# Kernel optimization log

Measured on AMD Instinct MI355X. Metric: run time of the kernel, lower is better.

## Reference

```python
import jax, jax.numpy as jnp
import numpy as np

T, B, N, C = 4, 16, 256, 512
H = 8
HID = 4 * C
TAU = 2.0
EPS = 1e-5
SCALE = 0.125

@jax.custom_vjp
def spike_fn(x):
    return (x >= 0.0).astype(x.dtype)

def _spike_fwd(x):
    return spike_fn(x), x

def _spike_bwd(x, g):
    alpha = 4.0  # spikingjelly sigmoid surrogate default
    s = jax.nn.sigmoid(alpha * x)
    return (g * alpha * s * (1.0 - s),)

spike_fn.defvjp(_spike_fwd, _spike_bwd)

def lif(x_seq, v_th=1.0):
    # Multi-step LIF: v += (x - v)/tau (decay_input, v_reset=0), hard reset, detach_reset
    def step(v, xt):
        v = v + (xt - v) / TAU
        s = spike_fn(v - v_th)
        v = v * (1.0 - jax.lax.stop_gradient(s))
        return v, s
    _, out = jax.lax.scan(step, jnp.zeros_like(x_seq[0]), x_seq)
    return out

def lin_bn(x2d, w, b, g, beta):
    # Linear then BatchNorm1d (training mode, per-channel stats over all rows).
    # BN on (TB, Cout, N) over (batch, N) == BN on flattened (TB*N, Cout) over axis 0.
    y = x2d @ w.T + b
    mu = jnp.mean(y, axis=0)
    var = jnp.var(y, axis=0)
    return g * (y - mu) * jax.lax.rsqrt(var + EPS) + beta

def setup_inputs() -> dict:
    key = jax.random.key(0)
    ks = jax.random.split(key, 10)
    d = {
        "x": jax.random.normal(ks[0], (T, B, N, C), jnp.float32),
        "s_x": jax.random.normal(ks[1], (T, B, N, C), jnp.float32),
    }
    def lin(k, cout, cin):
        return jax.random.normal(k, (cout, cin), jnp.float32) * 0.02
    d["qw"] = lin(ks[2], C, C); d["qb"] = jnp.zeros((C,), jnp.float32)
    d["qg"] = jnp.ones((C,), jnp.float32); d["qbeta"] = jnp.zeros((C,), jnp.float32)
    d["kw"] = lin(ks[3], C, C); d["kb"] = jnp.zeros((C,), jnp.float32)
    d["kg"] = jnp.ones((C,), jnp.float32); d["kbeta"] = jnp.zeros((C,), jnp.float32)
    d["vw"] = lin(ks[4], C, C); d["vb"] = jnp.zeros((C,), jnp.float32)
    d["vg"] = jnp.ones((C,), jnp.float32); d["vbeta"] = jnp.zeros((C,), jnp.float32)
    d["pw"] = lin(ks[5], C, C); d["pb"] = jnp.zeros((C,), jnp.float32)
    d["pg"] = jnp.ones((C,), jnp.float32); d["pbeta"] = jnp.zeros((C,), jnp.float32)
    d["f1w"] = lin(ks[6], HID, C); d["f1b"] = jnp.zeros((HID,), jnp.float32)
    d["f1g"] = jnp.ones((HID,), jnp.float32); d["f1beta"] = jnp.zeros((HID,), jnp.float32)
    d["f2w"] = lin(ks[7], C, HID); d["f2b"] = jnp.zeros((C,), jnp.float32)
    d["f2g"] = jnp.ones((C,), jnp.float32); d["f2beta"] = jnp.zeros((C,), jnp.float32)
    return d

def _block(x, s_x, qw, qb, qg, qbeta, kw, kb, kg, kbeta, vw, vb, vg, vbeta,
           pw, pb, pg, pbeta, f1w, f1b, f1g, f1beta, f2w, f2b, f2g, f2beta):
    Dh = C // H
    xf = x.reshape(T * B * N, C)
    # SSA (s_x is unused in the source forward)
    q = lif(lin_bn(xf, qw, qb, qg, qbeta).reshape(T, B, N, C))
    k = lif(lin_bn(xf, kw, kb, kg, kbeta).reshape(T, B, N, C))
    v = lin_bn(xf, vw, vb, vg, vbeta).reshape(T, B, N, C)  # v has no LIF in source
    q = q.reshape(T, B, N, H, Dh).transpose(0, 1, 3, 2, 4)  # tbhnd
    k = k.reshape(T, B, N, H, Dh).transpose(0, 1, 3, 2, 4)
    v = v.reshape(T, B, N, H, Dh).transpose(0, 1, 3, 2, 4)
    attn = jnp.einsum('tbhnd,tbhmd->tbhnm', q, k) * SCALE  # no softmax
    o = jnp.einsum('tbhnm,tbhmd->tbhnd', attn, v)
    o = o.transpose(0, 1, 3, 2, 4).reshape(T * B * N, C)
    o = lin_bn(o, pw, pb, pg, pbeta).reshape(T, B, N, C)
    x = x + o
    # MLP
    xf2 = x.reshape(T * B * N, C)
    h = lif(lin_bn(xf2, f1w, f1b, f1g, f1beta).reshape(T, B, N, HID))
    m = lif(lin_bn(h.reshape(T * B * N, HID), f2w, f2b, f2g, f2beta).reshape(T, B, N, C))
    return x + m

def reference(x, s_x, qw, qb, qg, qbeta, kw, kb, kg, kbeta, vw, vb, vg, vbeta,
              pw, pb, pg, pbeta, f1w, f1b, f1g, f1beta, f2w, f2b, f2g, f2beta):
    return _block(x, s_x, qw, qb, qg, qbeta, kw, kb, kg, kbeta, vw, vb, vg, vbeta,
                  pw, pb, pg, pbeta, f1w, f1b, f1g, f1beta, f2w, f2b, f2g, f2beta)
```

## Files before the change

kernel.cpp:

```cpp
#include <hip/hip_runtime.h>
#include <cstdint>

#define T_ 4
#define B_ 16
#define N_ 256
#define C_ 512
#define H_ 8
#define HID_ 2048
#define M_ (T_*B_*N_)
#define BNP_ (B_*N_)

__global__ __launch_bounds__(256, 2)
void gemm_f32_t128(const float* __restrict__ A, const float* __restrict__ W,
                   const float* __restrict__ bias, float* __restrict__ Y,
                   int Nc, int K) {
  __shared__ float As[2][16][132];
  __shared__ float Ws[2][16][132];
  const int tid  = threadIdx.x;
  const int row0 = blockIdx.y * 128;
  const int col0 = blockIdx.x * 128;
  const int tx = tid & 15, ty = tid >> 4;
  const int ar = tid >> 2;
  const int ac = (tid & 3) << 2;

  float acc[8][8];
  #pragma unroll
  for (int i = 0; i < 8; ++i)
    #pragma unroll
    for (int j = 0; j < 8; ++j) acc[i][j] = 0.f;

  const float* Ap0 = A + (size_t)(row0 + ar) * K + ac;
  const float* Ap1 = A + (size_t)(row0 + ar + 64) * K + ac;
  const float* Wp0 = W + (size_t)(col0 + ar) * K + ac;
  const float* Wp1 = W + (size_t)(col0 + ar + 64) * K + ac;

  float4 pa0 = *(const float4*)Ap0;
  float4 pa1 = *(const float4*)Ap1;
  float4 pw0 = *(const float4*)Wp0;
  float4 pw1 = *(const float4*)Wp1;
  As[0][ac+0][ar] = pa0.x; As[0][ac+1][ar] = pa0.y; As[0][ac+2][ar] = pa0.z; As[0][ac+3][ar] = pa0.w;
  As[0][ac+0][ar+64] = pa1.x; As[0][ac+1][ar+64] = pa1.y; As[0][ac+2][ar+64] = pa1.z; As[0][ac+3][ar+64] = pa1.w;
  Ws[0][ac+0][ar] = pw0.x; Ws[0][ac+1][ar] = pw0.y; Ws[0][ac+2][ar] = pw0.z; Ws[0][ac+3][ar] = pw0.w;
  Ws[0][ac+0][ar+64] = pw1.x; Ws[0][ac+1][ar+64] = pw1.y; Ws[0][ac+2][ar+64] = pw1.z; Ws[0][ac+3][ar+64] = pw1.w;
  __syncthreads();

  int buf = 0;
  for (int k0 = 0; k0 < K; k0 += 16) {
    const bool last = (k0 + 16 >= K);
    if (!last) {
      pa0 = *(const float4*)(Ap0 + k0 + 16);
      pa1 = *(const float4*)(Ap1 + k0 + 16);
      pw0 = *(const float4*)(Wp0 + k0 + 16);
      pw1 = *(const float4*)(Wp1 + k0 + 16);
    }
    #pragma unroll
    for (int kk = 0; kk < 16; ++kk) {
      float a[8], b[8];
      *(float4*)&a[0] = *(const float4*)&As[buf][kk][ty*4];
      *(float4*)&a[4] = *(const float4*)&As[buf][kk][64 + ty*4];
      *(float4*)&b[0] = *(const float4*)&Ws[buf][kk][tx*4];
      *(float4*)&b[4] = *(const float4*)&Ws[buf][kk][64 + tx*4];
      #pragma unroll
      for (int i = 0; i < 8; ++i)
        #pragma unroll
        for (int j = 0; j < 8; ++j)
          acc[i][j] = fmaf(a[i], b[j], acc[i][j]);
    }
    if (!last) {
      int nb = buf ^ 1;
      As[nb][ac+0][ar] = pa0.x; As[nb][ac+1][ar] = pa0.y; As[nb][ac+2][ar] = pa0.z; As[nb][ac+3][ar] = pa0.w;
      As[nb][ac+0][ar+64] = pa1.x; As[nb][ac+1][ar+64] = pa1.y; As[nb][ac+2][ar+64] = pa1.z; As[nb][ac+3][ar+64] = pa1.w;
      Ws[nb][ac+0][ar] = pw0.x; Ws[nb][ac+1][ar] = pw0.y; Ws[nb][ac+2][ar] = pw0.z; Ws[nb][ac+3][ar] = pw0.w;
      Ws[nb][ac+0][ar+64] = pw1.x; Ws[nb][ac+1][ar+64] = pw1.y; Ws[nb][ac+2][ar+64] = pw1.z; Ws[nb][ac+3][ar+64] = pw1.w;
      __syncthreads();
      buf = nb;
    }
  }

  #pragma unroll
  for (int ih = 0; ih < 2; ++ih)
    #pragma unroll
    for (int i = 0; i < 4; ++i) {
      size_t r = (size_t)(row0 + ih*64 + ty*4 + i);
      #pragma unroll
      for (int jh = 0; jh < 2; ++jh) {
        int c = col0 + jh*64 + tx*4;
        float4 o4;
        o4.x = acc[ih*4+i][jh*4+0] + bias[c+0];
        o4.y = acc[ih*4+i][jh*4+1] + bias[c+1];
        o4.z = acc[ih*4+i][jh*4+2] + bias[c+2];
        o4.w = acc[ih*4+i][jh*4+3] + bias[c+3];
        *(float4*)(Y + r * Nc + c) = o4;
      }
    }
}

__global__ __launch_bounds__(256)
void gemm_f32_t64x128(const float* __restrict__ A, const float* __restrict__ W,
                      const float* __restrict__ bias, float* __restrict__ Y,
                      int Nc, int K) {
  __shared__ float As[2][16][68];
  __shared__ float Ws[2][16][132];
  const int tid  = threadIdx.x;
  const int row0 = blockIdx.y * 64;
  const int col0 = blockIdx.x * 128;
  const int tx = tid & 15, ty = tid >> 4;
  const int ar = tid >> 2;
  const int ac = (tid & 3) << 2;

  float acc[4][8];
  #pragma unroll
  for (int i = 0; i < 4; ++i)
    #pragma unroll
    for (int j = 0; j < 8; ++j) acc[i][j] = 0.f;

  const float* Ap  = A + (size_t)(row0 + ar) * K + ac;
  const float* Wp0 = W + (size_t)(col0 + ar) * K + ac;
  const float* Wp1 = W + (size_t)(col0 + ar + 64) * K + ac;

  float4 pa  = *(const float4*)Ap;
  float4 pw0 = *(const float4*)Wp0;
  float4 pw1 = *(const float4*)Wp1;
  As[0][ac+0][ar] = pa.x; As[0][ac+1][ar] = pa.y; As[0][ac+2][ar] = pa.z; As[0][ac+3][ar] = pa.w;
  Ws[0][ac+0][ar] = pw0.x; Ws[0][ac+1][ar] = pw0.y; Ws[0][ac+2][ar] = pw0.z; Ws[0][ac+3][ar] = pw0.w;
  Ws[0][ac+0][ar+64] = pw1.x; Ws[0][ac+1][ar+64] = pw1.y; Ws[0][ac+2][ar+64] = pw1.z; Ws[0][ac+3][ar+64] = pw1.w;
  __syncthreads();

  int buf = 0;
  for (int k0 = 0; k0 < K; k0 += 16) {
    const bool last = (k0 + 16 >= K);
    if (!last) {
      pa  = *(const float4*)(Ap  + k0 + 16);
      pw0 = *(const float4*)(Wp0 + k0 + 16);
      pw1 = *(const float4*)(Wp1 + k0 + 16);
    }
    #pragma unroll
    for (int kk = 0; kk < 16; ++kk) {
      float4 av = *(const float4*)&As[buf][kk][ty*4];
      float b[8];
      *(float4*)&b[0] = *(const float4*)&Ws[buf][kk][tx*4];
      *(float4*)&b[4] = *(const float4*)&Ws[buf][kk][64 + tx*4];
      float a[4] = {av.x, av.y, av.z, av.w};
      #pragma unroll
      for (int i = 0; i < 4; ++i)
        #pragma unroll
        for (int j = 0; j < 8; ++j)
          acc[i][j] = fmaf(a[i], b[j], acc[i][j]);
    }
    if (!last) {
      int nb = buf ^ 1;
      As[nb][ac+0][ar] = pa.x; As[nb][ac+1][ar] = pa.y; As[nb][ac+2][ar] = pa.z; As[nb][ac+3][ar] = pa.w;
      Ws[nb][ac+0][ar] = pw0.x; Ws[nb][ac+1][ar] = pw0.y; Ws[nb][ac+2][ar] = pw0.z; Ws[nb][ac+3][ar] = pw0.w;
      Ws[nb][ac+0][ar+64] = pw1.x; Ws[nb][ac+1][ar+64] = pw1.y; Ws[nb][ac+2][ar+64] = pw1.z; Ws[nb][ac+3][ar+64] = pw1.w;
      __syncthreads();
      buf = nb;
    }
  }

  #pragma unroll
  for (int i = 0; i < 4; ++i) {
    size_t r = (size_t)(row0 + ty*4 + i);
    #pragma unroll
    for (int jh = 0; jh < 2; ++jh) {
      int c = col0 + jh*64 + tx*4;
      float4 o4;
      o4.x = acc[i][jh*4+0] + bias[c+0];
      o4.y = acc[i][jh*4+1] + bias[c+1];
      o4.z = acc[i][jh*4+2] + bias[c+2];
      o4.w = acc[i][jh*4+3] + bias[c+3];
      *(float4*)(Y + r * Nc + c) = o4;
    }
  }
}

__global__ __launch_bounds__(256)
void gemm_f64_v2(const float* __restrict__ A, const float* __restrict__ W,
                 const float* __restrict__ bias, float* __restrict__ Y,
                 int Nc, int K) {
  __shared__ double As[2][16][68];
  __shared__ double Ws[2][16][68];
  const int tid  = threadIdx.x;
  const int row0 = blockIdx.y * 64;
  const int col0 = blockIdx.x * 64;
  const int tx = tid & 15, ty = tid >> 4;
  const int lr = tid >> 2;
  const int lk = (tid & 3) << 2;

  double acc[4][4];
  #pragma unroll
  for (int i = 0; i < 4; ++i)
    #pragma unroll
    for (int j = 0; j < 4; ++j) acc[i][j] = 0.0;

  const float* Ap = A + (size_t)(row0 + lr) * K + lk;
  const float* Wp = W + (size_t)(col0 + lr) * K + lk;

  float4 pa = *(const float4*)Ap;
  float4 pw = *(const float4*)Wp;
  As[0][lk+0][lr] = (double)pa.x; As[0][lk+1][lr] = (double)pa.y;
  As[0][lk+2][lr] = (double)pa.z; As[0][lk+3][lr] = (double)pa.w;
  Ws[0][lk+0][lr] = (double)pw.x; Ws[0][lk+1][lr] = (double)pw.y;
  Ws[0][lk+2][lr] = (double)pw.z; Ws[0][lk+3][lr] = (double)pw.w;
  __syncthreads();

  int buf = 0;
  for (int k0 = 0; k0 < K; k0 += 16) {
    const bool last = (k0 + 16 >= K);
    if (!last) {
      pa = *(const float4*)(Ap + k0 + 16);
      pw = *(const float4*)(Wp + k0 + 16);
    }
    #pragma unroll
    for (int kk = 0; kk < 16; ++kk) {
      double a[4], b[4];
      *(double2*)&a[0] = *(const double2*)&As[buf][kk][ty*4];
      *(double2*)&a[2] = *(const double2*)&As[buf][kk][ty*4+2];
      *(double2*)&b[0] = *(const double2*)&Ws[buf][kk][tx*2];
      *(double2*)&b[2] = *(const double2*)&Ws[buf][kk][32 + tx*2];
      #pragma unroll
      for (int i = 0; i < 4; ++i)
        #pragma unroll
        for (int j = 0; j < 4; ++j)
          acc[i][j] = fma(a[i], b[j], acc[i][j]);
    }
    if (!last) {
      int nb = buf ^ 1;
      As[nb][lk+0][lr] = (double)pa.x; As[nb][lk+1][lr] = (double)pa.y;
      As[nb][lk+2][lr] = (double)pa.z; As[nb][lk+3][lr] = (double)pa.w;
      Ws[nb][lk+0][lr] = (double)pw.x; Ws[nb][lk+1][lr] = (double)pw.y;
      Ws[nb][lk+2][lr] = (double)pw.z; Ws[nb][lk+3][lr] = (double)pw.w;
      __syncthreads();
      buf = nb;
    }
  }

  #pragma unroll
  for (int i = 0; i < 4; ++i) {
    size_t r = (size_t)(row0 + ty*4 + i);
    int c0 = col0 + tx*2;
    float2 o0;
    o0.x = (float)(acc[i][0] + (double)bias[c0+0]);
    o0.y = (float)(acc[i][1] + (double)bias[c0+1]);
    *(float2*)(Y + r * Nc + c0) = o0;
    int c1 = col0 + 32 + tx*2;
    float2 o1;
    o1.x = (float)(acc[i][2] + (double)bias[c1+0]);
    o1.y = (float)(acc[i][3] + (double)bias[c1+1]);
    *(float2*)(Y + r * Nc + c1) = o1;
  }
}

__global__ __launch_bounds__(256)
void col_stats_partial(const float* __restrict__ Y, int Nc,
                       float* __restrict__ psum, float* __restrict__ psq) {
  const int r0 = blockIdx.x * 32;
  for (int c = threadIdx.x; c < Nc; c += 256) {
    float s = 0.f, q = 0.f;
    const float* p = Y + (size_t)r0 * Nc + c;
    for (int r = 0; r < 32; ++r) {
      float v = p[(size_t)r * Nc];
      s += v;
      q = fmaf(v, v, q);
    }
    psum[(size_t)blockIdx.x * Nc + c] = s;
    psq [(size_t)blockIdx.x * Nc + c] = q;
  }
}

__global__ void col_stats_final(const float* __restrict__ psum, const float* __restrict__ psq,
                                int Nc, const float* __restrict__ g, const float* __restrict__ beta,
                                float* __restrict__ chp) {
  int c = blockIdx.x * blockDim.x + threadIdx.x;
  if (c >= Nc) return;
  double s = 0.0, q = 0.0;
  for (int p = 0; p < 512; ++p) {
    s += (double)psum[(size_t)p * Nc + c];
    q += (double)psq [(size_t)p * Nc + c];
  }
  double mean = s / (double)M_;
  double var  = q / (double)M_ - mean * mean;
  float alpha = g[c] / sqrtf((float)var + 1e-5f);
  chp[2*c]   = alpha;
  chp[2*c+1] = fmaf(-(float)mean, alpha, beta[c]);
}

__global__ void col_stats_final_f64(const float* __restrict__ psum, const float* __restrict__ psq,
                                    int Nc, const float* __restrict__ g, const float* __restrict__ beta,
                                    double* __restrict__ chpd) {
  int c = blockIdx.x * blockDim.x + threadIdx.x;
  if (c >= Nc) return;
  double s = 0.0, q = 0.0;
  for (int p = 0; p < 512; ++p) {
    s += (double)psum[(size_t)p * Nc + c];
    q += (double)psq [(size_t)p * Nc + c];
  }
  double mean = s / (double)M_;
  double var  = q / (double)M_ - mean * mean;
  double alpha = (double)g[c] / sqrt(var + 1e-5);
  chpd[2*c]   = alpha;
  chpd[2*c+1] = (double)beta[c] - mean * alpha;
}

__global__ __launch_bounds__(256)
void bnlif_mask(const float* __restrict__ Y, const float* __restrict__ chp,
                unsigned long long* __restrict__ mask) {
  int lane = threadIdx.x & 63;
  int u  = blockIdx.x * 4 + (threadIdx.x >> 6);
  int bn = u >> 3, cg = u & 7;
  int c  = cg * 64 + lane;
  float alpha = chp[2*c], bb = chp[2*c+1];
  float v = 0.f;
  #pragma unroll
  for (int t = 0; t < 4; ++t) {
    float y  = Y[((size_t)(t * BNP_ + bn)) * C_ + c];
    float uu = fmaf(y, alpha, bb);
    v = v + (uu - v) * 0.5f;
    bool sp = (v >= 1.0f);
    unsigned long long m = __ballot(sp);
    if (sp) v = 0.f;
    if (lane == 0) mask[((size_t)(t * BNP_ + bn)) * H_ + cg] = m;
  }
}

__global__ void bn_apply_f64(const float* __restrict__ Y, const double* __restrict__ chpd,
                             float* __restrict__ out) {
  const long total4 = (long)M_ * C_ / 4;
  for (long i = (long)blockIdx.x * blockDim.x + threadIdx.x; i < total4;
       i += (long)gridDim.x * blockDim.x) {
    int c4 = (int)(i & (C_/4 - 1)) * 4;
    float4 y = ((const float4*)Y)[i];
    float4 r;
    r.x = (float)fma((double)y.x, chpd[2*(c4+0)], chpd[2*(c4+0)+1]);
    r.y = (float)fma((double)y.y, chpd[2*(c4+1)], chpd[2*(c4+1)+1]);
    r.z = (float)fma((double)y.z, chpd[2*(c4+2)], chpd[2*(c4+2)+1]);
    r.w = (float)fma((double)y.w, chpd[2*(c4+3)], chpd[2*(c4+3)+1]);
    ((float4*)out)[i] = r;
  }
}

__global__ void bn_residual_f64(const float* __restrict__ Y, const double* __restrict__ chpd,
                                const float* __restrict__ x, float* __restrict__ out) {
  const long total4 = (long)M_ * C_ / 4;
  for (long i = (long)blockIdx.x * blockDim.x + threadIdx.x; i < total4;
       i += (long)gridDim.x * blockDim.x) {
    int c4 = (int)(i & (C_/4 - 1)) * 4;
    float4 y = ((const float4*)Y)[i];
    float4 xv = ((const float4*)x)[i];
    float4 r;
    r.x = (float)((double)xv.x + fma((double)y.x, chpd[2*(c4+0)], chpd[2*(c4+0)+1]));
    r.y = (float)((double)xv.y + fma((double)y.y, chpd[2*(c4+1)], chpd[2*(c4+1)+1]));
    r.z = (float)((double)xv.z + fma((double)y.z, chpd[2*(c4+2)], chpd[2*(c4+2)+1]));
    r.w = (float)((double)xv.w + fma((double)y.w, chpd[2*(c4+3)], chpd[2*(c4+3)+1]));
    ((float4*)out)[i] = r;
  }
}

__global__ __launch_bounds__(256)
void bnlif_inplace(float* __restrict__ Y, const float* __restrict__ chp) {
  int c  = blockIdx.x * 256 + threadIdx.x;
  int bn = blockIdx.y;
  float alpha = chp[2*c], bb = chp[2*c+1];
  float v = 0.f;
  #pragma unroll
  for (int t = 0; t < 4; ++t) {
    size_t idx = ((size_t)(t * BNP_ + bn)) * HID_ + c;
    float uu = fmaf(Y[idx], alpha, bb);
    v = v + (uu - v) * 0.5f;
    bool sp = (v >= 1.f);
    Y[idx] = sp ? 1.f : 0.f;
    if (sp) v = 0.f;
  }
}

__global__ __launch_bounds__(256)
void bnlif_final(const float* __restrict__ Y, const float* __restrict__ chp,
                 const float* __restrict__ xo, float* __restrict__ out) {
  int c  = blockIdx.x * 256 + threadIdx.x;
  int bn = blockIdx.y;
  float alpha = chp[2*c], bb = chp[2*c+1];
  float v = 0.f;
  #pragma unroll
  for (int t = 0; t < 4; ++t) {
    size_t idx = ((size_t)(t * BNP_ + bn)) * C_ + c;
    float uu = fmaf(Y[idx], alpha, bb);
    v = v + (uu - v) * 0.5f;
    bool sp = (v >= 1.f);
    out[idx] = xo[idx] + (sp ? 1.f : 0.f);
    if (sp) v = 0.f;
  }
}

__global__ __launch_bounds__(256)
void attn_kernel_f64(const unsigned long long* __restrict__ qmask,
                     const unsigned long long* __restrict__ kmask,
                     const float* __restrict__ v, float* __restrict__ o) {
  __shared__ unsigned long long km[256];
  __shared__ float vt[256][64];
  int rb  = blockIdx.x & 3;
  int tbh = blockIdx.x >> 2;
  int h   = tbh & 7, tb = tbh >> 3;
  int tid = threadIdx.x;

  km[tid] = kmask[(size_t)(tb * 256 + tid) * H_ + h];
  const float* vbase = v + (size_t)tb * 256 * C_ + h * 64;
  #pragma unroll
  for (int i = 0; i < 16; ++i) {
    int f = i * 256 + tid;
    int r = f >> 4, c4 = f & 15;
    *(float4*)&vt[r][c4 * 4] = *(const float4*)(vbase + (size_t)r * C_ + c4 * 4);
  }
  int lane = tid & 63, w = tid >> 6;
  int nr = lane & 15, dg = lane >> 4;
  int n  = rb * 64 + w * 16 + nr;
  unsigned long long qm = qmask[(size_t)(tb * 256 + n) * H_ + h];
  __syncthreads();

  double acc[16];
  #pragma unroll
  for (int j = 0; j < 16; ++j) acc[j] = 0.0;

  for (int m = 0; m < 256; ++m) {
    double s = (double)__popcll(qm & km[m]) * 0.125;
    #pragma unroll
    for (int j = 0; j < 4; ++j) {
      float4 vv = *(const float4*)&vt[m][dg * 16 + j * 4];
      acc[j*4+0] = fma(s, (double)vv.x, acc[j*4+0]);
      acc[j*4+1] = fma(s, (double)vv.y, acc[j*4+1]);
      acc[j*4+2] = fma(s, (double)vv.z, acc[j*4+2]);
      acc[j*4+3] = fma(s, (double)vv.w, acc[j*4+3]);
    }
  }
  float* orow = o + (size_t)(tb * 256 + n) * C_ + h * 64 + dg * 16;
  #pragma unroll
  for (int j = 0; j < 4; ++j)
    *(float4*)(orow + j * 4) = make_float4((float)acc[j*4], (float)acc[j*4+1],
                                           (float)acc[j*4+2], (float)acc[j*4+3]);
}

extern "C" void kernel_launch(void* const* d_in, const int* in_sizes, int n_in,
                              void* d_out, int out_size, void* d_ws, size_t ws_size,
                              hipStream_t stream) {
  const float* x    = (const float*)d_in[0];
  const float* qw   = (const float*)d_in[2];
  const float* qb   = (const float*)d_in[3];
  const float* qg   = (const float*)d_in[4];
  const float* qbe  = (const float*)d_in[5];
  const float* kw   = (const float*)d_in[6];
  const float* kb   = (const float*)d_in[7];
  const float* kg   = (const float*)d_in[8];
  const float* kbe  = (const float*)d_in[9];
  const float* vw   = (const float*)d_in[10];
  const float* vb   = (const float*)d_in[11];
  const float* vg   = (const float*)d_in[12];
  const float* vbe  = (const float*)d_in[13];
  const float* pw   = (const float*)d_in[14];
  const float* pb   = (const float*)d_in[15];
  const float* pg   = (const float*)d_in[16];
  const float* pbe  = (const float*)d_in[17];
  const float* f1w  = (const float*)d_in[18];
  const float* f1b  = (const float*)d_in[19];
  const float* f1g  = (const float*)d_in[20];
  const float* f1be = (const float*)d_in[21];
  const float* f2w  = (const float*)d_in[22];
  const float* f2b  = (const float*)d_in[23];
  const float* f2g  = (const float*)d_in[24];
  const float* f2be = (const float*)d_in[25];

  char* ws = (char*)d_ws;
  float* bufY = (float*)(ws);
  float* bufV = (float*)(ws + 134217728ull);
  float* bufO = (float*)(ws + 167772160ull);
  unsigned long long* qmask = (unsigned long long*)(ws + 201326592ull);
  unsigned long long* kmask = (unsigned long long*)(ws + 202375168ull);
  float* psum = (float*)(ws + 203423744ull);
  float* psq  = (float*)(ws + 207618048ull);
  float* chp  = (float*)(ws + 211812352ull);
  double* chpd = (double*)(ws + 211828736ull);

  float* out = (float*)d_out;

  gemm_f32_t64x128<<<dim3(4,256), 256, 0, stream>>>(x, qw, qb, bufY, C_, C_);
  col_stats_partial<<<512, 256, 0, stream>>>(bufY, C_, psum, psq);
  col_stats_final<<<2, 256, 0, stream>>>(psum, psq, C_, qg, qbe, chp);
  bnlif_mask<<<8192, 256, 0, stream>>>(bufY, chp, qmask);
  gemm_f32_t64x128<<<dim3(4,256), 256, 0, stream>>>(x, kw, kb, bufY, C_, C_);
  col_stats_partial<<<512, 256, 0, stream>>>(bufY, C_, psum, psq);
  col_stats_final<<<2, 256, 0, stream>>>(psum, psq, C_, kg, kbe, chp);
  bnlif_mask<<<8192, 256, 0, stream>>>(bufY, chp, kmask);
  gemm_f64_v2<<<dim3(8,256), 256, 0, stream>>>(x, vw, vb, bufY, C_, C_);
  col_stats_partial<<<512, 256, 0, stream>>>(bufY, C_, psum, psq);
  col_stats_final_f64<<<2, 256, 0, stream>>>(psum, psq, C_, vg, vbe, chpd);
  bn_apply_f64<<<2048, 256, 0, stream>>>(bufY, chpd, bufV);
  attn_kernel_f64<<<2048, 256, 0, stream>>>(qmask, kmask, bufV, bufO);
  gemm_f64_v2<<<dim3(8,256), 256, 0, stream>>>(bufO, pw, pb, bufY, C_, C_);
  col_stats_partial<<<512, 256, 0, stream>>>(bufY, C_, psum, psq);
  col_stats_final_f64<<<2, 256, 0, stream>>>(psum, psq, C_, pg, pbe, chpd);
  bn_residual_f64<<<2048, 256, 0, stream>>>(bufY, chpd, x, bufO);
  gemm_f32_t128<<<dim3(16,128), 256, 0, stream>>>(bufO, f1w, f1b, bufY, HID_, C_);
  col_stats_partial<<<512, 256, 0, stream>>>(bufY, HID_, psum, psq);
  col_stats_final<<<8, 256, 0, stream>>>(psum, psq, HID_, f1g, f1be, chp);
  bnlif_inplace<<<dim3(8,4096), 256, 0, stream>>>(bufY, chp);
  gemm_f32_t64x128<<<dim3(4,256), 256, 0, stream>>>(bufY, f2w, f2b, bufV, C_, HID_);
  col_stats_partial<<<512, 256, 0, stream>>>(bufV, C_, psum, psq);
  col_stats_final<<<2, 256, 0, stream>>>(psum, psq, C_, f2g, f2be, chp);
  bnlif_final<<<dim3(2,4096), 256, 0, stream>>>(bufV, chp, bufO, out);
}
```

Measured before the change: 1.982 ms.

## Fuse Q/K projections into one GEMM and enlarge f64 and FC2 GEMM tiles

Q and K linear projections now run in a single kernel that loads each activation tile once and multiplies it against both weight matrices, writing two outputs. The f64 GEMM used for V and the projection is widened from a 64x64 to a 64x128 tile, and the FC2 GEMM moves to the 128x128 f32 kernel. The aim is to cut redundant activation reads and launches and raise arithmetic intensity. The cost is more registers and shared memory per block and fewer blocks, which can lower occupancy.

```diff
diff --git a/kernel.cpp b/kernel.cpp
--- a/kernel.cpp
+++ b/kernel.cpp
@@ -95,12 +95,15 @@
     }
 }
 
-__global__ __launch_bounds__(256)
-void gemm_f32_t64x128(const float* __restrict__ A, const float* __restrict__ W,
-                      const float* __restrict__ bias, float* __restrict__ Y,
-                      int Nc, int K) {
+__global__ __launch_bounds__(256, 2)
+void gemm_f32_qk(const float* __restrict__ A,
+                 const float* __restrict__ Wq, const float* __restrict__ bq,
+                 const float* __restrict__ Wk, const float* __restrict__ bk,
+                 float* __restrict__ Yq, float* __restrict__ Yk,
+                 int Nc, int K) {
   __shared__ float As[2][16][68];
-  __shared__ float Ws[2][16][132];
+  __shared__ float Wqs[2][16][132];
+  __shared__ float Wks[2][16][132];
   const int tid  = threadIdx.x;
   const int row0 = blockIdx.y * 64;
   const int col0 = blockIdx.x * 128;
@@ -108,22 +111,125 @@
   const int ar = tid >> 2;
   const int ac = (tid & 3) << 2;
 
-  float acc[4][8];
+  float accq[4][8], acck[4][8];
   #pragma unroll
   for (int i = 0; i < 4; ++i)
     #pragma unroll
-    for (int j = 0; j < 8; ++j) acc[i][j] = 0.f;
-
-  const float* Ap  = A + (size_t)(row0 + ar) * K + ac;
-  const float* Wp0 = W + (size_t)(col0 + ar) * K + ac;
-  const float* Wp1 = W + (size_t)(col0 + ar + 64) * K + ac;
+    for (int j = 0; j < 8; ++j) { accq[i][j] = 0.f; acck[i][j] = 0.f; }
+
+  const float* Ap   = A  + (size_t)(row0 + ar) * K + ac;
+  const float* Wqp0 = Wq + (size_t)(col0 + ar) * K + ac;
+  const float* Wqp1 = Wq + (size_t)(col0 + ar + 64) * K + ac;
+  const float* Wkp0 = Wk + (size_t)(col0 + ar) * K + ac;
+  const float* Wkp1 = Wk + (size_t)(col0 + ar + 64) * K + ac;
+
+  float4 pa  = *(const float4*)Ap;
+  float4 pq0 = *(const float4*)Wqp0;
+  float4 pq1 = *(const float4*)Wqp1;
+  float4 pk0 = *(const float4*)Wkp0;
+  float4 pk1 = *(const float4*)Wkp1;
+  As[0][ac+0][ar] = pa.x; As[0][ac+1][ar] = pa.y; As[0][ac+2][ar] = pa.z; As[0][ac+3][ar] = pa.w;
+  Wqs[0][ac+0][ar] = pq0.x; Wqs[0][ac+1][ar] = pq0.y; Wqs[0][ac+2][ar] = pq0.z; Wqs[0][ac+3][ar] = pq0.w;
+  Wqs[0][ac+0][ar+64] = pq1.x; Wqs[0][ac+1][ar+64] = pq1.y; Wqs[0][ac+2][ar+64] = pq1.z; Wqs[0][ac+3][ar+64] = pq1.w;
+  Wks[0][ac+0][ar] = pk0.x; Wks[0][ac+1][ar] = pk0.y; Wks[0][ac+2][ar] = pk0.z; Wks[0][ac+3][ar] = pk0.w;
+  Wks[0][ac+0][ar+64] = pk1.x; Wks[0][ac+1][ar+64] = pk1.y; Wks[0][ac+2][ar+64] = pk1.z; Wks[0][ac+3][ar+64] = pk1.w;
+  __syncthreads();
+
+  int buf = 0;
+  for (int k0 = 0; k0 < K; k0 += 16) {
+    const bool last = (k0 + 16 >= K);
+    if (!last) {
+      pa  = *(const float4*)(Ap   + k0 + 16);
+      pq0 = *(const float4*)(Wqp0 + k0 + 16);
+      pq1 = *(const float4*)(Wqp1 + k0 + 16);
+      pk0 = *(const float4*)(Wkp0 + k0 + 16);
+      pk1 = *(const float4*)(Wkp1 + k0 + 16);
+    }
+    #pragma unroll
+    for (int kk = 0; kk < 16; ++kk) {
+      float4 av = *(const float4*)&As[buf][kk][ty*4];
+      float a[4] = {av.x, av.y, av.z, av.w};
+      float b[8];
+      *(float4*)&b[0] = *(const float4*)&Wqs[buf][kk][tx*4];
+      *(float4*)&b[4] = *(const float4*)&Wqs[buf][kk][64 + tx*4];
+      #pragma unroll
+      for (int i = 0; i < 4; ++i)
+        #pragma unroll
+        for (int j = 0; j < 8; ++j)
+          accq[i][j] = fmaf(a[i], b[j], accq[i][j]);
+      *(float4*)&b[0] = *(const float4*)&Wks[buf][kk][tx*4];
+      *(float4*)&b[4] = *(const float4*)&Wks[buf][kk][64 + tx*4];
+      #pragma unroll
+      for (int i = 0; i < 4; ++i)
+        #pragma unroll
+        for (int j = 0; j < 8; ++j)
+          acck[i][j] = fmaf(a[i], b[j], acck[i][j]);
+    }
+    if (!last) {
+      int nb = buf ^ 1;
+      As[nb][ac+0][ar] = pa.x; As[nb][ac+1][ar] = pa.y; As[nb][ac+2][ar] = pa.z; As[nb][ac+3][ar] = pa.w;
+      Wqs[nb][ac+0][ar] = pq0.x; Wqs[nb][ac+1][ar] = pq0.y; Wqs[nb][ac+2][ar] = pq0.z; Wqs[nb][ac+3][ar] = pq0.w;
+      Wqs[nb][ac+0][ar+64] = pq1.x; Wqs[nb][ac+1][ar+64] = pq1.y; Wqs[nb][ac+2][ar+64] = pq1.z; Wqs[nb][ac+3][ar+64] = pq1.w;
+      Wks[nb][ac+0][ar] = pk0.x; Wks[nb][ac+1][ar] = pk0.y; Wks[nb][ac+2][ar] = pk0.z; Wks[nb][ac+3][ar] = pk0.w;
+      Wks[nb][ac+0][ar+64] = pk1.x; Wks[nb][ac+1][ar+64] = pk1.y; Wks[nb][ac+2][ar+64] = pk1.z; Wks[nb][ac+3][ar+64] = pk1.w;
+      __syncthreads();
+      buf = nb;
+    }
+  }
+
+  #pragma unroll
+  for (int i = 0; i < 4; ++i) {
+    size_t r = (size_t)(row0 + ty*4 + i);
+    #pragma unroll
+    for (int jh = 0; jh < 2; ++jh) {
+      int c = col0 + jh*64 + tx*4;
+      float4 oq, ok;
+      oq.x = accq[i][jh*4+0] + bq[c+0];
+      oq.y = accq[i][jh*4+1] + bq[c+1];
+      oq.z = accq[i][jh*4+2] + bq[c+2];
+      oq.w = accq[i][jh*4+3] + bq[c+3];
+      *(float4*)(Yq + r * Nc + c) = oq;
+      ok.x = acck[i][jh*4+0] + bk[c+0];
+      ok.y = acck[i][jh*4+1] + bk[c+1];
+      ok.z = acck[i][jh*4+2] + bk[c+2];
+      ok.w = acck[i][jh*4+3] + bk[c+3];
+      *(float4*)(Yk + r * Nc + c) = ok;
+    }
+  }
+}
+
+__global__ __launch_bounds__(256, 2)
+void gemm_f64_v3(const float* __restrict__ A, const float* __restrict__ W,
+                 const float* __restrict__ bias, float* __restrict__ Y,
+                 int Nc, int K) {
+  __shared__ double As[2][16][68];
+  __shared__ double Ws[2][16][132];
+  const int tid  = threadIdx.x;
+  const int row0 = blockIdx.y * 64;
+  const int col0 = blockIdx.x * 128;
+  const int tx = tid & 15, ty = tid >> 4;
+  const int lr = tid >> 2;
+  const int lk = (tid & 3) << 2;
+
+  double acc[4][8];
+  #pragma unroll
+  for (int i = 0; i < 4; ++i)
+    #pragma unroll
+    for (int j = 0; j < 8; ++j) acc[i][j] = 0.0;
+
+  const float* Ap  = A + (size_t)(row0 + lr) * K + lk;
+  const float* Wp0 = W + (size_t)(col0 + lr) * K + lk;
+  const float* Wp1 = W + (size_t)(col0 + lr + 64) * K + lk;
 
   float4 pa  = *(const float4*)Ap;
   float4 pw0 = *(const float4*)Wp0;
   float4 pw1 = *(const float4*)Wp1;
-  As[0][ac+0][ar] = pa.x; As[0][ac+1][ar] = pa.y; As[0][ac+2][ar] = pa.z; As[0][ac+3][ar] = pa.w;
-  Ws[0][ac+0][ar] = pw0.x; Ws[0][ac+1][ar] = pw0.y; Ws[0][ac+2][ar] = pw0.z; Ws[0][ac+3][ar] = pw0.w;
-  Ws[0][ac+0][ar+64] = pw1.x; Ws[0][ac+1][ar+64] = pw1.y; Ws[0][ac+2][ar+64] = pw1.z; Ws[0][ac+3][ar+64] = pw1.w;
+  As[0][lk+0][lr] = (double)pa.x; As[0][lk+1][lr] = (double)pa.y;
+  As[0][lk+2][lr] = (double)pa.z; As[0][lk+3][lr] = (double)pa.w;
+  Ws[0][lk+0][lr] = (double)pw0.x; Ws[0][lk+1][lr] = (double)pw0.y;
+  Ws[0][lk+2][lr] = (double)pw0.z; Ws[0][lk+3][lr] = (double)pw0.w;
+  Ws[0][lk+0][lr+64] = (double)pw1.x; Ws[0][lk+1][lr+64] = (double)pw1.y;
+  Ws[0][lk+2][lr+64] = (double)pw1.z; Ws[0][lk+3][lr+64] = (double)pw1.w;
   __syncthreads();
 
   int buf = 0;
@@ -136,99 +242,27 @@
     }
     #pragma unroll
     for (int kk = 0; kk < 16; ++kk) {
-      float4 av = *(const float4*)&As[buf][kk][ty*4];
-      float b[8];
-      *(float4*)&b[0] = *(const float4*)&Ws[buf][kk][tx*4];
-      *(float4*)&b[4] = *(const float4*)&Ws[buf][kk][64 + tx*4];
-      float a[4] = {av.x, av.y, av.z, av.w};
+      double a[4], b[8];
+      *(double2*)&a[0] = *(const double2*)&As[buf][kk][ty*4];
+      *(double2*)&a[2] = *(const double2*)&As[buf][kk][ty*4+2];
+      *(double2*)&b[0] = *(const double2*)&Ws[buf][kk][tx*2];
+      *(double2*)&b[2] = *(const double2*)&Ws[buf][kk][32 + tx*2];
+      *(double2*)&b[4] = *(const double2*)&Ws[buf][kk][64 + tx*2];
+      *(double2*)&b[6] = *(const double2*)&Ws[buf][kk][96 + tx*2];
       #pragma unroll
       for (int i = 0; i < 4; ++i)
         #pragma unroll
         for (int j = 0; j < 8; ++j)
-          acc[i][j] = fmaf(a[i], b[j], acc[i][j]);
-    }
-    if (!last) {
-      int nb = buf ^ 1;
-      As[nb][ac+0][ar] = pa.x; As[nb][ac+1][ar] = pa.y; As[nb][ac+2][ar] = pa.z; As[nb][ac+3][ar] = pa.w;
-      Ws[nb][ac+0][ar] = pw0.x; Ws[nb][ac+1][ar] = pw0.y; Ws[nb][ac+2][ar] = pw0.z; Ws[nb][ac+3][ar] = pw0.w;
-      Ws[nb][ac+0][ar+64] = pw1.x; Ws[nb][ac+1][ar+64] = pw1.y; Ws[nb][ac+2][ar+64] = pw1.z; Ws[nb][ac+3][ar+64] = pw1.w;
-      __syncthreads();
-      buf = nb;
-    }
-  }
-
-  #pragma unroll
-  for (int i = 0; i < 4; ++i) {
-    size_t r = (size_t)(row0 + ty*4 + i);
-    #pragma unroll
-    for (int jh = 0; jh < 2; ++jh) {
-      int c = col0 + jh*64 + tx*4;
-      float4 o4;
-      o4.x = acc[i][jh*4+0] + bias[c+0];
-      o4.y = acc[i][jh*4+1] + bias[c+1];
-      o4.z = acc[i][jh*4+2] + bias[c+2];
-      o4.w = acc[i][jh*4+3] + bias[c+3];
-      *(float4*)(Y + r * Nc + c) = o4;
-    }
-  }
-}
-
-__global__ __launch_bounds__(256)
-void gemm_f64_v2(const float* __restrict__ A, const float* __restrict__ W,
-                 const float* __restrict__ bias, float* __restrict__ Y,
-                 int Nc, int K) {
-  __shared__ double As[2][16][68];
-  __shared__ double Ws[2][16][68];
-  const int tid  = threadIdx.x;
-  const int row0 = blockIdx.y * 64;
-  const int col0 = blockIdx.x * 64;
-  const int tx = tid & 15, ty = tid >> 4;
-  const int lr = tid >> 2;
-  const int lk = (tid & 3) << 2;
-
-  double acc[4][4];
-  #pragma unroll
-  for (int i = 0; i < 4; ++i)
-    #pragma unroll
-    for (int j = 0; j < 4; ++j) acc[i][j] = 0.0;
-
-  const float* Ap = A + (size_t)(row0 + lr) * K + lk;
-  const float* Wp = W + (size_t)(col0 + lr) * K + lk;
-
-  float4 pa = *(const float4*)Ap;
-  float4 pw = *(const float4*)Wp;
-  As[0][lk+0][lr] = (double)pa.x; As[0][lk+1][lr] = (double)pa.y;
-  As[0][lk+2][lr] = (double)pa.z; As[0][lk+3][lr] = (double)pa.w;
-  Ws[0][lk+0][lr] = (double)pw.x; Ws[0][lk+1][lr] = (double)pw.y;
-  Ws[0][lk+2][lr] = (double)pw.z; Ws[0][lk+3][lr] = (double)pw.w;
-  __syncthreads();
-
-  int buf = 0;
-  for (int k0 = 0; k0 < K; k0 += 16) {
-    const bool last = (k0 + 16 >= K);
-    if (!last) {
-      pa = *(const float4*)(Ap + k0 + 16);
-      pw = *(const float4*)(Wp + k0 + 16);
-    }
-    #pragma unroll
-    for (int kk = 0; kk < 16; ++kk) {
-      double a[4], b[4];
-      *(double2*)&a[0] = *(const double2*)&As[buf][kk][ty*4];
-      *(double2*)&a[2] = *(const double2*)&As[buf][kk][ty*4+2];
-      *(double2*)&b[0] = *(const double2*)&Ws[buf][kk][tx*2];
-      *(double2*)&b[2] = *(const double2*)&Ws[buf][kk][32 + tx*2];
-      #pragma unroll
-      for (int i = 0; i < 4; ++i)
-        #pragma unroll
-        for (int j = 0; j < 4; ++j)
           acc[i][j] = fma(a[i], b[j], acc[i][j]);
     }
     if (!last) {
       int nb = buf ^ 1;
       As[nb][lk+0][lr] = (double)pa.x; As[nb][lk+1][lr] = (double)pa.y;
       As[nb][lk+2][lr] = (double)pa.z; As[nb][lk+3][lr] = (double)pa.w;
-      Ws[nb][lk+0][lr] = (double)pw.x; Ws[nb][lk+1][lr] = (double)pw.y;
-      Ws[nb][lk+2][lr] = (double)pw.z; Ws[nb][lk+3][lr] = (double)pw.w;
+      Ws[nb][lk+0][lr] = (double)pw0.x; Ws[nb][lk+1][lr] = (double)pw0.y;
+      Ws[nb][lk+2][lr] = (double)pw0.z; Ws[nb][lk+3][lr] = (double)pw0.w;
+      Ws[nb][lk+0][lr+64] = (double)pw1.x; Ws[nb][lk+1][lr+64] = (double)pw1.y;
+      Ws[nb][lk+2][lr+64] = (double)pw1.z; Ws[nb][lk+3][lr+64] = (double)pw1.w;
       __syncthreads();
       buf = nb;
     }
@@ -237,16 +271,14 @@
   #pragma unroll
   for (int i = 0; i < 4; ++i) {
     size_t r = (size_t)(row0 + ty*4 + i);
-    int c0 = col0 + tx*2;
-    float2 o0;
-    o0.x = (float)(acc[i][0] + (double)bias[c0+0]);
-    o0.y = (float)(acc[i][1] + (double)bias[c0+1]);
-    *(float2*)(Y + r * Nc + c0) = o0;
-    int c1 = col0 + 32 + tx*2;
-    float2 o1;
-    o1.x = (float)(acc[i][2] + (double)bias[c1+0]);
-    o1.y = (float)(acc[i][3] + (double)bias[c1+1]);
-    *(float2*)(Y + r * Nc + c1) = o1;
+    #pragma unroll
+    for (int g = 0; g < 4; ++g) {
+      int c = col0 + g*32 + tx*2;
+      float2 o2;
+      o2.x = (float)(acc[i][g*2+0] + (double)bias[c+0]);
+      o2.y = (float)(acc[i][g*2+1] + (double)bias[c+1]);
+      *(float2*)(Y + r * Nc + c) = o2;
+    }
   }
 }
 
@@ -468,6 +500,7 @@
 
   char* ws = (char*)d_ws;
   float* bufY = (float*)(ws);
+  float* bufK = bufY + 8388608;
   float* bufV = (float*)(ws + 134217728ull);
   float* bufO = (float*)(ws + 167772160ull);
   unsigned long long* qmask = (unsigned long long*)(ws + 201326592ull);
@@ -479,20 +512,19 @@
 
   float* out = (float*)d_out;
 
-  gemm_f32_t64x128<<<dim3(4,256), 256, 0, stream>>>(x, qw, qb, bufY, C_, C_);
+  gemm_f32_qk<<<dim3(4,256), 256, 0, stream>>>(x, qw, qb, kw, kb, bufY, bufK, C_, C_);
   col_stats_partial<<<512, 256, 0, stream>>>(bufY, C_, psum, psq);
   col_stats_final<<<2, 256, 0, stream>>>(psum, psq, C_, qg, qbe, chp);
   bnlif_mask<<<8192, 256, 0, stream>>>(bufY, chp, qmask);
-  gemm_f32_t64x128<<<dim3(4,256), 256, 0, stream>>>(x, kw, kb, bufY, C_, C_);
-  col_stats_partial<<<512, 256, 0, stream>>>(bufY, C_, psum, psq);
+  col_stats_partial<<<512, 256, 0, stream>>>(bufK, C_, psum, psq);
   col_stats_final<<<2, 256, 0, stream>>>(psum, psq, C_, kg, kbe, chp);
-  bnlif_mask<<<8192, 256, 0, stream>>>(bufY, chp, kmask);
-  gemm_f64_v2<<<dim3(8,256), 256, 0, stream>>>(x, vw, vb, bufY, C_, C_);
+  bnlif_mask<<<8192, 256, 0, stream>>>(bufK, chp, kmask);
+  gemm_f64_v3<<<dim3(4,256), 256, 0, stream>>>(x, vw, vb, bufY, C_, C_);
   col_stats_partial<<<512, 256, 0, stream>>>(bufY, C_, psum, psq);
   col_stats_final_f64<<<2, 256, 0, stream>>>(psum, psq, C_, vg, vbe, chpd);
   bn_apply_f64<<<2048, 256, 0, stream>>>(bufY, chpd, bufV);
   attn_kernel_f64<<<2048, 256, 0, stream>>>(qmask, kmask, bufV, bufO);
-  gemm_f64_v2<<<dim3(8,256), 256, 0, stream>>>(bufO, pw, pb, bufY, C_, C_);
+  gemm_f64_v3<<<dim3(4,256), 256, 0, stream>>>(bufO, pw, pb, bufY, C_, C_);
   col_stats_partial<<<512, 256, 0, stream>>>(bufY, C_, psum, psq);
   col_stats_final_f64<<<2, 256, 0, stream>>>(psum, psq, C_, pg, pbe, chpd);
   bn_residual_f64<<<2048, 256, 0, stream>>>(bufY, chpd, x, bufO);
@@ -500,7 +532,7 @@
   col_stats_partial<<<512, 256, 0, stream>>>(bufY, HID_, psum, psq);
   col_stats_final<<<8, 256, 0, stream>>>(psum, psq, HID_, f1g, f1be, chp);
   bnlif_inplace<<<dim3(8,4096), 256, 0, stream>>>(bufY, chp);
-  gemm_f32_t64x128<<<dim3(4,256), 256, 0, stream>>>(bufY, f2w, f2b, bufV, C_, HID_);
+  gemm_f32_t128<<<dim3(4,128), 256, 0, stream>>>(bufY, f2w, f2b, bufV, C_, HID_);
   col_stats_partial<<<512, 256, 0, stream>>>(bufV, C_, psum, psq);
   col_stats_final<<<2, 256, 0, stream>>>(psum, psq, C_, f2g, f2be, chp);
   bnlif_final<<<dim3(2,4096), 256, 0, stream>>>(bufV, chp, bufO, out);
```

Measured after the change: 1.937 ms. -2.3%, faster.
